# Optimization experiments

Measured on AMD Instinct MI355X. Metric: run time of the kernel, lower is better.

Reference implementation:

```python
import jax, jax.numpy as jnp
import numpy as np


def setup_inputs() -> dict:
    key = jax.random.key(0)
    ks = jax.random.split(key, 7)
    B, I, H = 8192, 1024, 1024
    x = jax.random.normal(ks[0], (B, I), dtype=jnp.float32)
    h_prev = jax.random.normal(ks[1], (B, H), dtype=jnp.float32)
    C_prev = jax.random.normal(ks[2], (B, H), dtype=jnp.float32)
    W_f = jax.random.normal(ks[3], (I + H, H), dtype=jnp.float32) * 0.01
    W_i = jax.random.normal(ks[4], (I + H, H), dtype=jnp.float32) * 0.01
    W_C = jax.random.normal(ks[5], (I + H, H), dtype=jnp.float32) * 0.01
    W_o = jax.random.normal(ks[6], (I + H, H), dtype=jnp.float32) * 0.01
    b = jnp.zeros((H,), dtype=jnp.float32)
    return {"x": x, "h_prev": h_prev, "C_prev": C_prev,
            "W_f": W_f, "b_f": b, "W_i": W_i, "b_i": b,
            "W_C": W_C, "b_C": b, "W_o": W_o, "b_o": b}


def reference(x, h_prev, C_prev, W_f, b_f, W_i, b_i, W_C, b_C, W_o, b_o):
    combined = jnp.concatenate([x, h_prev], axis=1)  # [B, I+H]
    # Fuse the four gate GEMMs into one [B, I+H] x [I+H, 4H] matmul.
    W = jnp.concatenate([W_f, W_i, W_o, W_C], axis=1)  # [I+H, 4H]
    b = jnp.concatenate([b_f, b_i, b_o, b_C], axis=0)  # [4H]
    gates = combined @ W + b                            # [B, 4H]
    H = C_prev.shape[1]
    f_t = jax.nn.sigmoid(gates[:, 0:H])
    i_t = jax.nn.sigmoid(gates[:, H:2 * H])
    o_t = jax.nn.sigmoid(gates[:, 2 * H:3 * H])
    C_tilda = jnp.tanh(gates[:, 3 * H:4 * H])
    C_t = f_t * C_prev + i_t * C_tilda
    h_t = o_t * jnp.tanh(C_t)
    return (h_t, C_t)
```

## Files before the change

### kernel.cpp

```cpp
#include <hip/hip_runtime.h>
#include <hip/hip_bf16.h>

#define B_SZ 8192
#define IH   2048
#define H_SZ 1024
#define BM   256
#define BK   64
#define NT   (IH / BK)
#define NI   (NT / 2)
#define DBUF 65536
#define WOFF 32768

typedef __attribute__((ext_vector_type(8))) short  short8;
typedef __attribute__((ext_vector_type(4))) float  floatx4;

static __device__ __forceinline__ ushort f2bf(float f) {
  union { float f; unsigned u; } v; v.f = f;
  unsigned u = v.u;
  u += 0x7fffu + ((u >> 16) & 1u);
  return (ushort)(u >> 16);
}
static __device__ __forceinline__ float sigmoidf_(float x) {
  return 1.0f / (1.0f + __expf(-x));
}
static __device__ __forceinline__ float tanhf_(float x) {
  float ax = fabsf(x);
  float e = __expf(-2.0f * ax);
  float t = (1.0f - e) / (1.0f + e);
  return copysignf(t, x);
}
static __device__ __forceinline__ void gload_lds16(const void* gsrc, void* ldst) {
  __builtin_amdgcn_global_load_lds(
      (__attribute__((address_space(1))) const void*)gsrc,
      (__attribute__((address_space(3))) void*)ldst, 16, 0, 0);
}

__global__ __launch_bounds__(256) void convert_w_kernel(
    const float* __restrict__ Wf, const float* __restrict__ Wi,
    const float* __restrict__ Wo, const float* __restrict__ Wc,
    ushort* __restrict__ Wt) {
  __shared__ float tile[64][65];
  const int g  = blockIdx.z;
  const float* W = (g == 0) ? Wf : (g == 1) ? Wi : (g == 2) ? Wo : Wc;
  const int n0 = blockIdx.x * 64;
  const int k0 = blockIdx.y * 64;
  const int tid = threadIdx.x;
#pragma unroll
  for (int i = 0; i < 4; ++i) {
    int c = i * 256 + tid;
    int r = c >> 4, c4 = c & 15;
    float4 v = *(const float4*)(W + (size_t)(k0 + r) * H_SZ + n0 + c4 * 4);
    tile[r][c4 * 4 + 0] = v.x;
    tile[r][c4 * 4 + 1] = v.y;
    tile[r][c4 * 4 + 2] = v.z;
    tile[r][c4 * 4 + 3] = v.w;
  }
  __syncthreads();
  const int n  = tid >> 2;
  const int kc = (tid & 3) * 16;
  ushort o[16] __attribute__((aligned(16)));
#pragma unroll
  for (int e = 0; e < 16; ++e) o[e] = f2bf(tile[kc + e][n]);
  ushort* dst = Wt + ((size_t)g * H_SZ + n0 + n) * IH + k0 + kc;
  *(uint4*)(dst)     = *(uint4*)&o[0];
  *(uint4*)(dst + 8) = *(uint4*)&o[8];
}

__global__ __launch_bounds__(256) void convert_a_kernel(
    const float* __restrict__ x, const float* __restrict__ hp,
    ushort* __restrict__ Abf) {
  size_t idx = ((size_t)blockIdx.x * 256 + threadIdx.x) * 8;
  size_t row = idx >> 11;
  size_t col = idx & 2047;
  const float* src = (col < 1024) ? (x  + row * 1024 + col)
                                  : (hp + row * 1024 + (col - 1024));
  float4 v0 = *(const float4*)(src);
  float4 v1 = *(const float4*)(src + 4);
  ushort o[8] __attribute__((aligned(16)));
  o[0] = f2bf(v0.x); o[1] = f2bf(v0.y); o[2] = f2bf(v0.z); o[3] = f2bf(v0.w);
  o[4] = f2bf(v1.x); o[5] = f2bf(v1.y); o[6] = f2bf(v1.z); o[7] = f2bf(v1.w);
  *(uint4*)(Abf + idx) = *(uint4*)&o[0];
}

__global__ __launch_bounds__(512, 2) void lstm_fused_kernel(
    const float* __restrict__ Cp, const ushort* __restrict__ Wt,
    const ushort* __restrict__ Abf,
    const float* __restrict__ bf_, const float* __restrict__ bi_,
    const float* __restrict__ bo_, const float* __restrict__ bc_,
    float* __restrict__ out) {
  __shared__ char lds[2 * DBUF];

  const int bid = blockIdx.x;
  const int wg  = (bid & 7) * 64 + (bid >> 3);
  const int b0  = (wg >> 4) * BM;
  const int n0g = (wg & 15) * 64;

  const int tid = threadIdx.x;
  const int ln  = tid & 63;
  const int wv  = tid >> 6;
  const int wm  = wv >> 1, wn = wv & 1;

  floatx4 acc[4][8];
#pragma unroll
  for (int m = 0; m < 4; ++m)
#pragma unroll
    for (int j = 0; j < 8; ++j) acc[m][j] = {0.f, 0.f, 0.f, 0.f};

  const int sw  = (ln & 7) << 4;
  const int kb0 = (((ln >> 4) << 4)) ^ sw;
  const int kb1 = (64 + ((ln >> 4) << 4)) ^ sw;
  const int aR  = (wm * 64 + (ln & 15)) * 128;
  const int bR  = WOFF + (wn * 32 + (ln & 15)) * 128;
  int aB0[2], aB1[2], bB0[2], bB1[2];
#pragma unroll
  for (int d = 0; d < 2; ++d) {
    aB0[d] = d * DBUF + aR + kb0;  aB1[d] = d * DBUF + aR + kb1;
    bB0[d] = d * DBUF + bR + kb0;  bB1[d] = d * DBUF + bR + kb1;
  }

  const int    kcsw = ((tid & 7) * 16) ^ (((tid >> 3) & 7) << 4);
  const char*  AbfB = (const char*)Abf;
  const char*  WtB  = (const char*)Wt;
  size_t aoff[2];
#pragma unroll
  for (int i = 0; i < 2; ++i)
    aoff[i] = ((size_t)(b0 + i * 64 + (tid >> 3)) << 12) + kcsw;
  size_t woff[2][2];
#pragma unroll
  for (int h = 0; h < 2; ++h)
#pragma unroll
    for (int i = 0; i < 2; ++i) {
      int nrt  = h * 128 + i * 64 + (tid >> 3);
      int g    = nrt >> 6, nloc = nrt & 63;
      woff[h][i] = ((size_t)(g * H_SZ + n0g + nloc) << 12) + kcsw;
    }
  int dsto[2];
#pragma unroll
  for (int i = 0; i < 2; ++i) dsto[i] = (i * 512 + wv * 64) * 16;

#define STAGE_A(db, ktb, h)                                                   \
  do {                                                                        \
    gload_lds16(AbfB + aoff[0] + ((size_t)(h) << 19) + (ktb),                 \
                lds + (db) + (h) * 16384 + dsto[0]);                          \
    gload_lds16(AbfB + aoff[1] + ((size_t)(h) << 19) + (ktb),                 \
                lds + (db) + (h) * 16384 + dsto[1]);                          \
  } while (0)
#define STAGE_W(db, ktb, h)                                                   \
  do {                                                                        \
    gload_lds16(WtB + woff[h][0] + (ktb),                                     \
                lds + (db) + WOFF + (h) * 16384 + dsto[0]);                   \
    gload_lds16(WtB + woff[h][1] + (ktb),                                     \
                lds + (db) + WOFF + (h) * 16384 + dsto[1]);                   \
  } while (0)

  short8 aF[4][2];
  short8 bF[8][2];
#define RD_A(dbi, mf)                                                         \
  do {                                                                        \
    aF[mf][0] = *(const short8*)(lds + aB0[dbi] + (mf) * 2048);               \
    aF[mf][1] = *(const short8*)(lds + aB1[dbi] + (mf) * 2048);               \
  } while (0)
#define RD_B(dbi, j)                                                          \
  do {                                                                        \
    bF[j][0] = *(const short8*)(lds + bB0[dbi] + ((j) >> 1) * 8192 +          \
                                ((j) & 1) * 2048);                            \
    bF[j][1] = *(const short8*)(lds + bB1[dbi] + ((j) >> 1) * 8192 +          \
                                ((j) & 1) * 2048);                            \
  } while (0)
#define MFQ(mh, jh)                                                           \
  do {                                                                        \
    __builtin_amdgcn_s_setprio(1);                                            \
    _Pragma("unroll")                                                         \
    for (int k_ = 0; k_ < 2; ++k_)                                            \
      _Pragma("unroll")                                                       \
      for (int mf_ = 2 * (mh); mf_ < 2 * (mh) + 2; ++mf_)                     \
        _Pragma("unroll")                                                     \
        for (int j_ = 4 * (jh); j_ < 4 * (jh) + 4; ++j_)                      \
          acc[mf_][j_] = __builtin_amdgcn_mfma_f32_16x16x32_bf16(             \
              aF[mf_][k_], bF[j_][k_], acc[mf_][j_], 0, 0, 0);                \
    __builtin_amdgcn_s_setprio(0);                                            \
  } while (0)
#define BAR   __builtin_amdgcn_s_barrier()
#define VMC6  asm volatile("s_waitcnt vmcnt(6)" ::: "memory")

  STAGE_W(0, 0, 0); STAGE_A(0, 0, 0); STAGE_A(0, 0, 1); STAGE_W(0, 0, 1);
  STAGE_W(DBUF, 128, 0); STAGE_A(DBUF, 128, 0); STAGE_A(DBUF, 128, 1);
  VMC6;
  BAR;

#pragma unroll 1
  for (int it = 0; it < NI; ++it) {
    const int kt1b  = (2 * it + 1) * 128;
    const int ktn0b = ((2 * it + 2) & 31) * 128;
    const int ktn1b = ((2 * it + 3) & 31) * 128;
    RD_A(0, 0); RD_A(0, 1);
    RD_B(0, 0); RD_B(0, 1); RD_B(0, 2); RD_B(0, 3);
    STAGE_W(DBUF, kt1b, 1);
    BAR; MFQ(0, 0); BAR;
    RD_A(0, 2); RD_A(0, 3);
    STAGE_W(0, ktn0b, 0);
    BAR; MFQ(1, 0); BAR;
    RD_B(0, 4); RD_B(0, 5); RD_B(0, 6); RD_B(0, 7);
    STAGE_A(0, ktn0b, 0);
    BAR; MFQ(0, 1); BAR;
    STAGE_A(0, ktn0b, 1);
    BAR; MFQ(1, 1);
    VMC6; BAR;
    RD_A(1, 0); RD_A(1, 1);
    RD_B(1, 0); RD_B(1, 1); RD_B(1, 2); RD_B(1, 3);
    STAGE_W(0, ktn0b, 1);
    BAR; MFQ(0, 0); BAR;
    RD_A(1, 2); RD_A(1, 3);
    STAGE_W(DBUF, ktn1b, 0);
    BAR; MFQ(1, 0); BAR;
    RD_B(1, 4); RD_B(1, 5); RD_B(1, 6); RD_B(1, 7);
    STAGE_A(DBUF, ktn1b, 0);
    BAR; MFQ(0, 1); BAR;
    STAGE_A(DBUF, ktn1b, 1);
    BAR; MFQ(1, 1);
    VMC6; BAR;
  }

  const int colq = ln & 15;
  const int rq   = ln >> 4;
  float* outh = out;
  float* outC = out + (size_t)B_SZ * H_SZ;
#pragma unroll
  for (int mf = 0; mf < 4; ++mf) {
#pragma unroll
    for (int ns = 0; ns < 2; ++ns) {
      int n = n0g + wn * 32 + ns * 16 + colq;
      float vbf = bf_[n], vbi = bi_[n], vbo = bo_[n], vbc = bc_[n];
#pragma unroll
      for (int r = 0; r < 4; ++r) {
        int row = b0 + wm * 64 + mf * 16 + rq * 4 + r;
        float fg = sigmoidf_(acc[mf][0 + ns][r] + vbf);
        float ig = sigmoidf_(acc[mf][2 + ns][r] + vbi);
        float og = sigmoidf_(acc[mf][4 + ns][r] + vbo);
        float cg = tanhf_  (acc[mf][6 + ns][r] + vbc);
        float cp = Cp[(size_t)row * H_SZ + n];
        float Ct = fg * cp + ig * cg;
        float ht = og * tanhf_(Ct);
        outh[(size_t)row * H_SZ + n] = ht;
        outC[(size_t)row * H_SZ + n] = Ct;
      }
    }
  }
#undef STAGE_A
#undef STAGE_W
#undef RD_A
#undef RD_B
#undef MFQ
#undef BAR
#undef VMC6
}

extern "C" void kernel_launch(void* const* d_in, const int* in_sizes, int n_in,
                              void* d_out, int out_size, void* d_ws, size_t ws_size,
                              hipStream_t stream) {
  const float* x  = (const float*)d_in[0];
  const float* hp = (const float*)d_in[1];
  const float* Cp = (const float*)d_in[2];
  const float* Wf = (const float*)d_in[3];
  const float* bf = (const float*)d_in[4];
  const float* Wi = (const float*)d_in[5];
  const float* bi = (const float*)d_in[6];
  const float* Wc = (const float*)d_in[7];
  const float* bc = (const float*)d_in[8];
  const float* Wo = (const float*)d_in[9];
  const float* bo = (const float*)d_in[10];

  ushort* Wt  = (ushort*)d_ws;
  ushort* Abf = (ushort*)((char*)d_ws + (16u << 20));

  dim3 gridT(16, 32, 4);
  convert_w_kernel<<<gridT, 256, 0, stream>>>(Wf, Wi, Wo, Wc, Wt);
  convert_a_kernel<<<8192, 256, 0, stream>>>(x, hp, Abf);

  lstm_fused_kernel<<<512, 512, 0, stream>>>(Cp, Wt, Abf,
                                             bf, bi, bo, bc, (float*)d_out);
}
```

Measured before the change: 158.5 us.

## Restructure GEMM main loop into half-phases with fewer barriers and 32-bit offsets

Reorganizes the double-buffered bf16 MFMA loop so each phase reads all four A fragments and half of the B fragments, then issues 16 MFMAs per block instead of 8. This halves the number of barrier-separated phases per iteration and regroups the global-to-LDS stage issues, with adjusted vmcnt waits. It also switches global offsets from size_t to 32-bit unsigned to cut 64-bit address arithmetic. The risks are higher register pressure from holding more fragments live and possible LDS hazards if the new staging order overwrites buffers that are still being read.

```diff
diff --git a/kernel.cpp b/kernel.cpp
--- a/kernel.cpp
+++ b/kernel.cpp
@@ -118,21 +118,21 @@
     bB0[d] = d * DBUF + bR + kb0;  bB1[d] = d * DBUF + bR + kb1;
   }
 
-  const int    kcsw = ((tid & 7) * 16) ^ (((tid >> 3) & 7) << 4);
+  const unsigned kcsw = ((tid & 7) * 16) ^ (((tid >> 3) & 7) << 4);
   const char*  AbfB = (const char*)Abf;
   const char*  WtB  = (const char*)Wt;
-  size_t aoff[2];
+  unsigned aoff[2];
 #pragma unroll
   for (int i = 0; i < 2; ++i)
-    aoff[i] = ((size_t)(b0 + i * 64 + (tid >> 3)) << 12) + kcsw;
-  size_t woff[2][2];
+    aoff[i] = ((unsigned)(b0 + i * 64 + (tid >> 3)) << 12) + kcsw;
+  unsigned woff[2][2];
 #pragma unroll
   for (int h = 0; h < 2; ++h)
 #pragma unroll
     for (int i = 0; i < 2; ++i) {
       int nrt  = h * 128 + i * 64 + (tid >> 3);
       int g    = nrt >> 6, nloc = nrt & 63;
-      woff[h][i] = ((size_t)(g * H_SZ + n0g + nloc) << 12) + kcsw;
+      woff[h][i] = ((unsigned)(g * H_SZ + n0g + nloc) << 12) + kcsw;
     }
   int dsto[2];
 #pragma unroll
@@ -140,16 +140,16 @@
 
 #define STAGE_A(db, ktb, h)                                                   \
   do {                                                                        \
-    gload_lds16(AbfB + aoff[0] + ((size_t)(h) << 19) + (ktb),                 \
+    gload_lds16(AbfB + (aoff[0] + ((unsigned)(h) << 19) + (unsigned)(ktb)),   \
                 lds + (db) + (h) * 16384 + dsto[0]);                          \
-    gload_lds16(AbfB + aoff[1] + ((size_t)(h) << 19) + (ktb),                 \
+    gload_lds16(AbfB + (aoff[1] + ((unsigned)(h) << 19) + (unsigned)(ktb)),   \
                 lds + (db) + (h) * 16384 + dsto[1]);                          \
   } while (0)
 #define STAGE_W(db, ktb, h)                                                   \
   do {                                                                        \
-    gload_lds16(WtB + woff[h][0] + (ktb),                                     \
+    gload_lds16(WtB + (woff[h][0] + (unsigned)(ktb)),                         \
                 lds + (db) + WOFF + (h) * 16384 + dsto[0]);                   \
-    gload_lds16(WtB + woff[h][1] + (ktb),                                     \
+    gload_lds16(WtB + (woff[h][1] + (unsigned)(ktb)),                         \
                 lds + (db) + WOFF + (h) * 16384 + dsto[1]);                   \
   } while (0)
 
@@ -167,13 +167,16 @@
     bF[j][1] = *(const short8*)(lds + bB1[dbi] + ((j) >> 1) * 8192 +          \
                                 ((j) & 1) * 2048);                            \
   } while (0)
-#define MFQ(mh, jh)                                                           \
+#define RDQA(d)  do { RD_A(d, 0); RD_A(d, 1); RD_A(d, 2); RD_A(d, 3); } while (0)
+#define RDB03(d) do { RD_B(d, 0); RD_B(d, 1); RD_B(d, 2); RD_B(d, 3); } while (0)
+#define RDB47(d) do { RD_B(d, 4); RD_B(d, 5); RD_B(d, 6); RD_B(d, 7); } while (0)
+#define MFQ(jh)                                                               \
   do {                                                                        \
     __builtin_amdgcn_s_setprio(1);                                            \
     _Pragma("unroll")                                                         \
     for (int k_ = 0; k_ < 2; ++k_)                                            \
       _Pragma("unroll")                                                       \
-      for (int mf_ = 2 * (mh); mf_ < 2 * (mh) + 2; ++mf_)                     \
+      for (int mf_ = 0; mf_ < 4; ++mf_)                                       \
         _Pragma("unroll")                                                     \
         for (int j_ = 4 * (jh); j_ < 4 * (jh) + 4; ++j_)                      \
           acc[mf_][j_] = __builtin_amdgcn_mfma_f32_16x16x32_bf16(             \
@@ -181,11 +184,11 @@
     __builtin_amdgcn_s_setprio(0);                                            \
   } while (0)
 #define BAR   __builtin_amdgcn_s_barrier()
-#define VMC6  asm volatile("s_waitcnt vmcnt(6)" ::: "memory")
+#define VMC(n) asm volatile("s_waitcnt vmcnt(" #n ")" ::: "memory")
 
   STAGE_W(0, 0, 0); STAGE_A(0, 0, 0); STAGE_A(0, 0, 1); STAGE_W(0, 0, 1);
   STAGE_W(DBUF, 128, 0); STAGE_A(DBUF, 128, 0); STAGE_A(DBUF, 128, 1);
-  VMC6;
+  VMC(6);
   BAR;
 
 #pragma unroll 1
@@ -193,32 +196,18 @@
     const int kt1b  = (2 * it + 1) * 128;
     const int ktn0b = ((2 * it + 2) & 31) * 128;
     const int ktn1b = ((2 * it + 3) & 31) * 128;
-    RD_A(0, 0); RD_A(0, 1);
-    RD_B(0, 0); RD_B(0, 1); RD_B(0, 2); RD_B(0, 3);
+    RDQA(0); RDB03(0);
     STAGE_W(DBUF, kt1b, 1);
-    BAR; MFQ(0, 0); BAR;
-    RD_A(0, 2); RD_A(0, 3);
-    STAGE_W(0, ktn0b, 0);
-    BAR; MFQ(1, 0); BAR;
-    RD_B(0, 4); RD_B(0, 5); RD_B(0, 6); RD_B(0, 7);
-    STAGE_A(0, ktn0b, 0);
-    BAR; MFQ(0, 1); BAR;
-    STAGE_A(0, ktn0b, 1);
-    BAR; MFQ(1, 1);
-    VMC6; BAR;
-    RD_A(1, 0); RD_A(1, 1);
-    RD_B(1, 0); RD_B(1, 1); RD_B(1, 2); RD_B(1, 3);
-    STAGE_W(0, ktn0b, 1);
-    BAR; MFQ(0, 0); BAR;
-    RD_A(1, 2); RD_A(1, 3);
-    STAGE_W(DBUF, ktn1b, 0);
-    BAR; MFQ(1, 0); BAR;
-    RD_B(1, 4); RD_B(1, 5); RD_B(1, 6); RD_B(1, 7);
-    STAGE_A(DBUF, ktn1b, 0);
-    BAR; MFQ(0, 1); BAR;
-    STAGE_A(DBUF, ktn1b, 1);
-    BAR; MFQ(1, 1);
-    VMC6; BAR;
+    BAR; MFQ(0); BAR;
+    RDB47(0);
+    STAGE_W(0, ktn0b, 0); STAGE_A(0, ktn0b, 0);
+    BAR; MFQ(1); VMC(4); BAR;
+    RDQA(1); RDB03(1);
+    STAGE_A(0, ktn0b, 1); STAGE_W(0, ktn0b, 1);
+    BAR; MFQ(0); BAR;
+    RDB47(1);
+    STAGE_W(DBUF, ktn1b, 0); STAGE_A(DBUF, ktn1b, 0); STAGE_A(DBUF, ktn1b, 1);
+    BAR; MFQ(1); VMC(6); BAR;
   }
 
   const int colq = ln & 15;
@@ -250,9 +239,12 @@
 #undef STAGE_W
 #undef RD_A
 #undef RD_B
+#undef RDQA
+#undef RDB03
+#undef RDB47
 #undef MFQ
 #undef BAR
-#undef VMC6
+#undef VMC
 }
 
 extern "C" void kernel_launch(void* const* d_in, const int* in_sizes, int n_in,
```

After: 157.8 us. No clear change (-0.4%).
